# Performance work log

Measured on AMD Instinct MI355X. Metric: run time of the kernel, lower is better.

## Reference

```python
import jax, jax.numpy as jnp
import numpy as np

C = 512
GROUPS = 32
EPS = 1e-5  # torch GroupNorm default


def setup_inputs() -> dict:
    key = jax.random.key(0)
    ks = jax.random.split(key, 11)
    B, H, W = 4, 64, 64
    s = 1.0 / np.sqrt(C)
    inp = {
        "x": jax.random.normal(ks[0], (B, C, H, W), dtype=jnp.float32),
        "gn_scale": jnp.ones((C,), jnp.float32),
        "gn_bias": jnp.zeros((C,), jnp.float32),
        "wq": jax.random.normal(ks[1], (C, C), jnp.float32) * s,
        "bq": jax.random.normal(ks[2], (C,), jnp.float32) * 0.01,
        "wk": jax.random.normal(ks[3], (C, C), jnp.float32) * s,
        "bk": jax.random.normal(ks[4], (C,), jnp.float32) * 0.01,
        "wv": jax.random.normal(ks[5], (C, C), jnp.float32) * s,
        "bv": jax.random.normal(ks[6], (C,), jnp.float32) * 0.01,
        "wo": jax.random.normal(ks[7], (C, C), jnp.float32) * s,
        "bo": jax.random.normal(ks[8], (C,), jnp.float32) * 0.01,
    }
    return inp


def group_norm(x, scale, bias):
    # x: [B, C, H, W]; normalize within each of GROUPS channel groups over (C/G, H, W)
    B, Cc, H, W = x.shape
    xg = x.reshape(B, GROUPS, Cc // GROUPS, H, W)
    mean = jnp.mean(xg, axis=(2, 3, 4), keepdims=True)
    var = jnp.var(xg, axis=(2, 3, 4), keepdims=True)
    xg = (xg - mean) * jax.lax.rsqrt(var + EPS)
    xn = xg.reshape(B, Cc, H, W)
    return xn * scale[None, :, None, None] + bias[None, :, None, None]


def reference(x, gn_scale, gn_bias, wq, bq, wk, bk, wv, bv, wo, bo):
    B, Cc, H, W = x.shape
    h = group_norm(x, gn_scale, gn_bias)
    # 1x1 convs == channel matmuls; work in [B, HW, C] layout
    hf = h.reshape(B, Cc, H * W).transpose(0, 2, 1)  # [B, N, C]
    q = hf @ wq.T + bq                               # [B, N, C]
    k = hf @ wk.T + bk
    v = hf @ wv.T + bv
    scale = jnp.asarray(Cc, x.dtype) ** -0.5
    attn = jnp.einsum("bnc,bmc->bnm", q, k) * scale  # [B, N, N]
    attn = jax.nn.softmax(attn, axis=-1)
    o = jnp.einsum("bnm,bmc->bnc", attn, v)          # [B, N, C]
    o = o @ wo.T + bo
    o = o.transpose(0, 2, 1).reshape(B, Cc, H, W)
    return x + o
```

## Files before the change

### kernel.cpp

```cpp
#include <hip/hip_runtime.h>
#include <cstdint>
#include <cstddef>

typedef unsigned short ushort_t;
typedef __attribute__((ext_vector_type(8))) __bf16 bf16x8;
typedef __attribute__((ext_vector_type(4))) float f32x4;

#define DEVINL __device__ __forceinline__

DEVINL ushort_t f2bf(float f) {
  union { __bf16 b; ushort_t u; } v;
  v.b = (__bf16)f;
  return v.u;
}
DEVINL float bf2f(ushort_t u) {
  union { unsigned u; float f; } v; v.u = ((unsigned)u) << 16;
  return v.f;
}

DEVINL float wred_sum(float x) {
#pragma unroll
  for (int o = 32; o > 0; o >>= 1) x += __shfl_xor(x, o, 64);
  return x;
}

DEVINL void async16(ushort_t* lds, const ushort_t* g) {
  __builtin_amdgcn_global_load_lds(
      (__attribute__((address_space(1))) const unsigned int*)g,
      (__attribute__((address_space(3))) unsigned int*)lds, 16, 0, 0);
}

template <int CPR>
DEVINL int fswz(int r) {
  if constexpr (CPR == 4) return (r >> 2) & 3;
  else return r & 7;
}

__global__ __launch_bounds__(256) void gn_stats_k(const float* __restrict__ x,
                                                  float* __restrict__ stats) {
  const int bg = blockIdx.x;
  const float4* base = (const float4*)(x + ((size_t)bg << 16));
  float s = 0.f, q = 0.f;
  for (int i = threadIdx.x; i < 16384; i += 256) {
    float4 f = base[i];
    s += f.x + f.y + f.z + f.w;
    q += f.x * f.x + f.y * f.y + f.z * f.z + f.w * f.w;
  }
  s = wred_sum(s);
  q = wred_sum(q);
  __shared__ float rs[4], rq[4];
  const int lane = threadIdx.x & 63, wid = threadIdx.x >> 6;
  if (lane == 0) { rs[wid] = s; rq[wid] = q; }
  __syncthreads();
  if (threadIdx.x == 0) {
    float S = rs[0] + rs[1] + rs[2] + rs[3];
    float Q = rq[0] + rq[1] + rq[2] + rq[3];
    float mean = S * (1.f / 65536.f);
    float var = Q * (1.f / 65536.f) - mean * mean;
    stats[2 * bg] = mean;
    stats[2 * bg + 1] = rsqrtf(var + 1e-5f);
  }
}

__global__ __launch_bounds__(256) void gn_apply_k(const float* __restrict__ x,
                                                  const float* __restrict__ stats,
                                                  const float* __restrict__ gs,
                                                  const float* __restrict__ gb,
                                                  ushort_t* __restrict__ h) {
  __shared__ ushort_t tile[32][33];
  const int bid = blockIdx.x;
  const int b = bid >> 11;
  const int r = bid & 2047;
  const int ct = r >> 7, nt = r & 127;
  const int c0 = ct << 5, n0 = nt << 5;
  const int tx = threadIdx.x & 31, ty = threadIdx.x >> 5;
#pragma unroll
  for (int i = 0; i < 4; ++i) {
    const int c = c0 + ty + i * 8;
    const float mean = stats[2 * (b * 32 + (c >> 4))];
    const float rstd = stats[2 * (b * 32 + (c >> 4)) + 1];
    const float xv = x[(((size_t)b * 512 + c) << 12) + n0 + tx];
    tile[ty + i * 8][tx] = f2bf((xv - mean) * rstd * gs[c] + gb[c]);
  }
  __syncthreads();
#pragma unroll
  for (int i = 0; i < 4; ++i) {
    const int n = n0 + ty + i * 8;
    h[(((size_t)b << 12) + n) * 512 + c0 + tx] = tile[tx][ty + i * 8];
  }
}

struct Ptr4 { const float* src[4]; float wsc[4]; };
__global__ __launch_bounds__(256) void cvt_all_k(Ptr4 s, ushort_t* __restrict__ dst) {
  const int i = blockIdx.x * 256 + threadIdx.x;
  const int m = i >> 18;
  dst[i] = f2bf(s.src[m][i & 262143] * s.wsc[m]);
}

struct Ptr3 { const float* bias[3]; ushort_t* out[3]; float bs[3]; };

template <int BM, int BN, int BK, int EPI>
__global__ __launch_bounds__(256) void gemm_nt_k(
    const ushort_t* __restrict__ A, int lda, const ushort_t* __restrict__ Bm, int ldb,
    void* __restrict__ Cout, int ldc, const float* __restrict__ bias,
    const float* __restrict__ resid, float scale, int K,
    size_t azs, size_t bzs, size_t czs, Ptr3 p3, float* __restrict__ lbuf) {
  constexpr int CPR = BK / 8;
  constexpr int WTM = BM / 2, WTN = BN / 2;
  constexpr int MI = WTM / 16, NI = WTN / 16;
  constexpr int AR = (BM * CPR) / 256;
  constexpr int BR = (BN * CPR) / 256;
  __shared__ ushort_t Als[BM * BK];
  __shared__ ushort_t Bls[BN * BK];
  const int tid = threadIdx.x;
  const int lane = tid & 63;
  const int wid = tid >> 6;
  const int quad = lane >> 4;
  const int r16 = lane & 15;
  const int wm = wid >> 1, wn = wid & 1;
  const int m0 = blockIdx.y * BM;
  const int n0 = blockIdx.x * BN;
  const int zb = blockIdx.z;

  A += azs * zb;
  Bm += bzs * zb;

  f32x4 acc[MI][NI] = {};

  for (int kt = 0; kt < K; kt += BK) {
#pragma unroll
    for (int r = 0; r < AR; ++r) {
      const int s = r * 256 + tid;
      const int row = s / CPR;
      const int q = (s % CPR) ^ fswz<CPR>(row);
      async16(&Als[s << 3], A + (size_t)(m0 + row) * lda + kt + (q << 3));
    }
#pragma unroll
    for (int r = 0; r < BR; ++r) {
      const int s = r * 256 + tid;
      const int row = s / CPR;
      const int q = (s % CPR) ^ fswz<CPR>(row);
      async16(&Bls[s << 3], Bm + (size_t)(n0 + row) * ldb + kt + (q << 3));
    }
    __syncthreads();
#pragma unroll
    for (int kf = 0; kf < BK / 32; ++kf) {
      bf16x8 af[MI], bfr[NI];
#pragma unroll
      for (int mi = 0; mi < MI; ++mi) {
        const int lr = wm * WTM + mi * 16 + r16;
        const int ch = kf * 4 + quad;
        af[mi] = *reinterpret_cast<const bf16x8*>(
            &Als[(lr * CPR + (ch ^ fswz<CPR>(lr))) << 3]);
      }
#pragma unroll
      for (int ni = 0; ni < NI; ++ni) {
        const int lr = wn * WTN + ni * 16 + r16;
        const int ch = kf * 4 + quad;
        bfr[ni] = *reinterpret_cast<const bf16x8*>(
            &Bls[(lr * CPR + (ch ^ fswz<CPR>(lr))) << 3]);
      }
#pragma unroll
      for (int mi = 0; mi < MI; ++mi)
#pragma unroll
        for (int ni = 0; ni < NI; ++ni)
          acc[mi][ni] = __builtin_amdgcn_mfma_f32_16x16x32_bf16(
              af[mi], bfr[ni], acc[mi][ni], 0, 0, 0);
    }
    __syncthreads();
  }

  const int mrow = m0 + wm * WTM;
  const int ncol = n0 + wn * WTN;
  if constexpr (EPI == 2) {
    float* C = (float*)Cout;
#pragma unroll
    for (int ni = 0; ni < NI; ++ni) {
      const int col = ncol + ni * 16 + r16;
      const float bvv = bias[col];
#pragma unroll
      for (int mi = 0; mi < MI; ++mi) {
        const int rowb = mrow + mi * 16 + quad * 4;
        const int bb = rowb >> 12;
        const int nl = rowb & 4095;
        const size_t base = (((size_t)bb * 512 + col) << 12) + nl;
        const float4 rv = *(const float4*)&resid[base];
        float4 ov;
        ov.x = rv.x + acc[mi][ni][0] + bvv;
        ov.y = rv.y + acc[mi][ni][1] + bvv;
        ov.z = rv.z + acc[mi][ni][2] + bvv;
        ov.w = rv.w + acc[mi][ni][3] + bvv;
        *(float4*)&C[base] = ov;
      }
    }
  } else if constexpr (EPI == 3) {
    const float* bz = p3.bias[zb];
    const float bsc = p3.bs[zb];
    ushort_t* O = p3.out[zb];
    if (zb < 2) {
#pragma unroll
      for (int ni = 0; ni < NI; ++ni) {
        const int col = ncol + ni * 16 + r16;
        const float bvv = bz[col] * bsc;
#pragma unroll
        for (int mi = 0; mi < MI; ++mi) {
          const int rowb = mrow + mi * 16 + quad * 4;
#pragma unroll
          for (int rr = 0; rr < 4; ++rr)
            O[(size_t)(rowb + rr) * 512 + col] = f2bf(acc[mi][ni][rr] + bvv);
        }
      }
    } else {
#pragma unroll
      for (int ni = 0; ni < NI; ++ni) {
        const int col = ncol + ni * 16 + r16;
        const float bvv = bz[col];
#pragma unroll
        for (int mi = 0; mi < MI; ++mi) {
          const int rowb = mrow + mi * 16 + quad * 4;
          const int bb = rowb >> 12;
          const int nn = rowb & 4095;
          ushort4 pk;
          pk.x = f2bf(acc[mi][ni][0] + bvv);
          pk.y = f2bf(acc[mi][ni][1] + bvv);
          pk.z = f2bf(acc[mi][ni][2] + bvv);
          pk.w = f2bf(acc[mi][ni][3] + bvv);
          *(ushort4*)&O[(((size_t)bb * 512 + col) << 12) + nn] = pk;
        }
      }
    }
  }
}

template <int BM, int BN, int WGM, int WGN, int EPI>
__global__ __launch_bounds__(512, 2) void gemm8p_k(
    const ushort_t* __restrict__ A, int lda,
    const ushort_t* __restrict__ Bm, int ldb,
    void* __restrict__ Cout, int ldc, int K,
    size_t azs, size_t bzs, size_t czs, float* __restrict__ lbuf) {
  constexpr int WTM = BM / WGM, WTN = BN / WGN;
  constexpr int MI = WTM / 16, NI = WTN / 16;
  constexpr int MH = MI / 2, NH = NI / 2;
  constexpr int ALD = BM / 64;
  constexpr int BLD = BN / 64;
  constexpr int TOT = ALD + BLD;
  constexpr int VMC = TOT / 4;
  constexpr int AHALF = BM * 64;
  constexpr int HALF = (BM + BN) * 64;

  extern __shared__ ushort_t lds8[];
  const int tid = threadIdx.x;
  const int lane = tid & 63;
  const int quad = lane >> 4;
  const int r16 = lane & 15;
  const int wid = tid >> 6;
  const int wm = wid / WGN, wn = wid % WGN;

  int bx, by, bz;
  {
    const int flat = blockIdx.x + (EPI == 4 ? 16 : 4) * (blockIdx.y + 16 * blockIdx.z);
    if constexpr (EPI == 4) {
      const int xcd = flat & 7, s = flat >> 3;
      const int w = s & 31, half = w >> 4, idx = w & 15;
      bx = (xcd & 3) * 4 + (idx & 3);
      by = ((xcd >> 2) + 2 * half) * 4 + (idx >> 2);
      bz = s >> 5;
    } else {
      const int xcd = flat & 7, s = flat >> 3;
      bx = s & 3;
      const int yz = xcd + (s >> 2) * 8;
      by = yz & 15; bz = yz >> 4;
    }
  }
  const int m0 = by * BM, n0 = bx * BN, zb = bz;
  A += azs * zb;
  Bm += bzs * zb;
  const int NT = K >> 6;

  const ushort_t* src[TOT];
  ushort_t* dst[TOT];
#pragma unroll
  for (int l = 0; l < TOT; ++l) {
    const bool isA = l < ALD;
    const int li = isA ? l : l - ALD;
    const int s = li * 512 + tid;
    const int row = s >> 3;
    const int q = (s & 7) ^ (row & 7);
    src[l] = (isA ? A + (size_t)(m0 + row) * lda
                  : Bm + (size_t)(n0 + row) * ldb) + (q << 3);
    dst[l] = lds8 + (isA ? 0 : AHALF) + (s << 3);
  }

  f32x4 acc[MI][NI] = {};

#pragma unroll
  for (int l = 0; l < TOT; ++l) async16(dst[l], src[l]);

  bf16x8 afq[MH][2], bfq[NH][2];

#pragma unroll 2
  for (int t = 0; t < NT; ++t) {
    const int nbuf = (t + 1) & 1;
    const ushort_t* Ab = lds8 + (t & 1) * HALF;
    const ushort_t* Bb = Ab + AHALF;
    const int koff = ((t + 1 < NT) ? t + 1 : NT - 1) << 6;

#define STAGEG(G)                                                              \
    { constexpr int S_ = ((G) * TOT) / 4, E_ = (((G) + 1) * TOT) / 4;          \
      _Pragma("unroll")                                                        \
      for (int l = S_; l < E_; ++l) async16(dst[l] + nbuf * HALF, src[l] + koff); }

#define LOADA(MHh)                                                             \
    _Pragma("unroll") for (int i = 0; i < MH; ++i)                             \
    _Pragma("unroll") for (int kf = 0; kf < 2; ++kf) {                         \
      const int lr = wm * WTM + ((MHh) * MH + i) * 16 + r16;                   \
      const int cc = (kf * 4 + quad) ^ (lr & 7);                               \
      afq[i][kf] = *reinterpret_cast<const bf16x8*>(&Ab[lr * 64 + cc * 8]); }

#define LOADB(NHh)                                                             \
    _Pragma("unroll") for (int j = 0; j < NH; ++j)                             \
    _Pragma("unroll") for (int kf = 0; kf < 2; ++kf) {                         \
      const int lr = wn * WTN + ((NHh) * NH + j) * 16 + r16;                   \
      const int cc = (kf * 4 + quad) ^ (lr & 7);                               \
      bfq[j][kf] = *reinterpret_cast<const bf16x8*>(&Bb[lr * 64 + cc * 8]); }

#define MMAQ(MHh, NHh)                                                         \
    __builtin_amdgcn_s_setprio(1);                                             \
    _Pragma("unroll") for (int i = 0; i < MH; ++i)                             \
    _Pragma("unroll") for (int j = 0; j < NH; ++j)                             \
    _Pragma("unroll") for (int kf = 0; kf < 2; ++kf)                           \
      acc[(MHh) * MH + i][(NHh) * NH + j] =                                    \
          __builtin_amdgcn_mfma_f32_16x16x32_bf16(                             \
              afq[i][kf], bfq[j][kf], acc[(MHh) * MH + i][(NHh) * NH + j],     \
              0, 0, 0);                                                        \
    __builtin_amdgcn_s_setprio(0);

    STAGEG(0)
    asm volatile("s_waitcnt vmcnt(%0)" :: "i"(VMC) : "memory");
    __builtin_amdgcn_s_barrier();
    __builtin_amdgcn_sched_barrier(0);
    LOADA(0)
    LOADB(0)
    MMAQ(0, 0)
    __builtin_amdgcn_sched_barrier(0);
    __builtin_amdgcn_s_barrier();
    STAGEG(1)
    LOADB(1)
    MMAQ(0, 1)
    __builtin_amdgcn_sched_barrier(0);
    __builtin_amdgcn_s_barrier();
    STAGEG(2)
    LOADA(1)
    MMAQ(1, 1)
    __builtin_amdgcn_sched_barrier(0);
    __builtin_amdgcn_s_barrier();
    STAGEG(3)
    LOADB(0)
    MMAQ(1, 0)
    __builtin_amdgcn_sched_barrier(0);
    __builtin_amdgcn_s_barrier();
#undef STAGEG
#undef LOADA
#undef LOADB
#undef MMAQ
  }

  const int mrow = m0 + wm * WTM;
  const int ncol = n0 + wn * WTN;
  if constexpr (EPI == 4) {
    ushort_t* C = (ushort_t*)Cout + czs * zb;
    float* Lz = lbuf + (size_t)zb * 4096;
#pragma unroll
    for (int mi = 0; mi < MI; ++mi) {
#pragma unroll
      for (int rr = 0; rr < 4; ++rr) {
        const int row = mrow + mi * 16 + quad * 4 + rr;
        float ps = 0.f;
#pragma unroll
        for (int ni = 0; ni < NI; ++ni) {
          const int col = ncol + ni * 16 + r16;
          const ushort_t ub = f2bf(__expf(acc[mi][ni][rr]));
          C[(size_t)row * ldc + col] = ub;
          ps += bf2f(ub);
        }
#pragma unroll
        for (int o = 1; o < 16; o <<= 1) ps += __shfl_xor(ps, o, 64);
        if (r16 == 0) atomicAdd(&Lz[row], ps);
      }
    }
  } else {
    ushort_t* C = (ushort_t*)Cout + czs * zb;
    const float* Lz = lbuf + (size_t)zb * 4096;
#pragma unroll
    for (int mi = 0; mi < MI; ++mi) {
#pragma unroll
      for (int rr = 0; rr < 4; ++rr) {
        const int row = mrow + mi * 16 + quad * 4 + rr;
        const float inv = 1.f / Lz[row];
#pragma unroll
        for (int ni = 0; ni < NI; ++ni) {
          const int col = ncol + ni * 16 + r16;
          C[(size_t)row * ldc + col] = f2bf(acc[mi][ni][rr] * inv);
        }
      }
    }
  }
}

extern "C" void kernel_launch(void* const* d_in, const int* in_sizes, int n_in,
                              void* d_out, int out_size, void* d_ws, size_t ws_size,
                              hipStream_t stream) {
  const float* x  = (const float*)d_in[0];
  const float* gs = (const float*)d_in[1];
  const float* gb = (const float*)d_in[2];
  const float* wq = (const float*)d_in[3];
  const float* bq = (const float*)d_in[4];
  const float* wk = (const float*)d_in[5];
  const float* bk = (const float*)d_in[6];
  const float* wv = (const float*)d_in[7];
  const float* bv = (const float*)d_in[8];
  const float* wo = (const float*)d_in[9];
  const float* bo = (const float*)d_in[10];
  float* out = (float*)d_out;

  const size_t HNC = (size_t)4 * 4096 * 512;
  char* w = (char*)d_ws;
  float* stats  = (float*)w;    w += 4096;
  float* Ls     = (float*)w;    w += (size_t)4 * 4096 * 4;
  ushort_t* wb  = (ushort_t*)w; w += (size_t)4 * 262144 * 2;
  ushort_t* h   = (ushort_t*)w; w += HNC * 2;
  ushort_t* q   = (ushort_t*)w; w += HNC * 2;
  ushort_t* kk  = (ushort_t*)w; w += HNC * 2;
  ushort_t* vt  = (ushort_t*)w; w += HNC * 2;
  ushort_t* Se  = (ushort_t*)w; w += (size_t)4 * 4096 * 4096 * 2;

  const float sc = 0.044194173824159216f;

  static bool attr_done = false;
  if (!attr_done) {
    (void)hipFuncSetAttribute((const void*)gemm8p_k<256, 256, 2, 4, 4>,
                              hipFuncAttributeMaxDynamicSharedMemorySize, 131072);
    (void)hipFuncSetAttribute((const void*)gemm8p_k<256, 128, 4, 2, 5>,
                              hipFuncAttributeMaxDynamicSharedMemorySize, 98304);
    attr_done = true;
  }

  gn_stats_k<<<128, 256, 0, stream>>>(x, stats);
  gn_apply_k<<<8192, 256, 0, stream>>>(x, stats, gs, gb, h);
  Ptr4 wsrc;
  wsrc.src[0] = wq; wsrc.src[1] = wk; wsrc.src[2] = wv; wsrc.src[3] = wo;
  wsrc.wsc[0] = sc; wsrc.wsc[1] = 1.f; wsrc.wsc[2] = 1.f; wsrc.wsc[3] = 1.f;
  cvt_all_k<<<4096, 256, 0, stream>>>(wsrc, wb);
  hipMemsetAsync(Ls, 0, (size_t)4 * 4096 * 4, stream);

  Ptr3 qkv;
  qkv.bias[0] = bq; qkv.bias[1] = bk; qkv.bias[2] = bv;
  qkv.out[0] = q; qkv.out[1] = kk; qkv.out[2] = vt;
  qkv.bs[0] = sc; qkv.bs[1] = 1.f; qkv.bs[2] = 1.f;
  gemm_nt_k<128, 128, 32, 3><<<dim3(4, 128, 3), 256, 0, stream>>>(
      h, 512, wb, 512, nullptr, 0, nullptr, nullptr, 1.f, 512,
      0, 262144, 0, qkv, nullptr);

  gemm8p_k<256, 256, 2, 4, 4><<<dim3(16, 16, 4), 512, 131072, stream>>>(
      q, 512, kk, 512, Se, 4096, 512,
      (size_t)4096 * 512, (size_t)4096 * 512, (size_t)4096 * 4096, Ls);
  gemm8p_k<256, 128, 4, 2, 5><<<dim3(4, 16, 4), 512, 98304, stream>>>(
      Se, 4096, vt, 4096, h, 512, 4096,
      (size_t)4096 * 4096, (size_t)512 * 4096, (size_t)4096 * 512, Ls);

  Ptr3 e0{};
  gemm_nt_k<128, 128, 32, 2><<<dim3(4, 128, 1), 256, 0, stream>>>(
      h, 512, wb + (size_t)3 * 262144, 512, out, 512, bo, x, 1.f, 512,
      0, 0, 0, e0, nullptr);
}
```

Before: 394.7 us.

## Compute softmax row sums via ones-MFMA in PV GEMM, drop atomics and memset

The softmax denominator is no longer accumulated with per-row atomicAdds in the QK^T epilogue. Instead the PV GEMM runs extra MFMAs against a vector of ones to sum the exp'd bf16 scores per row, and the memset and L buffer go away. The finely staged 4-phase ping-pong main loop with partial vmcnt waits is also replaced by a simpler loop: full vmcnt/lgkmcnt wait, one barrier per K-step, all B fragments held in registers. This removes atomic traffic but adds MFMA work and register pressure, and may lose the latency hiding the old staged schedule provided.

```diff
diff --git a/kernel.cpp b/kernel.cpp
--- a/kernel.cpp
+++ b/kernel.cpp
@@ -104,7 +104,7 @@
     const ushort_t* __restrict__ A, int lda, const ushort_t* __restrict__ Bm, int ldb,
     void* __restrict__ Cout, int ldc, const float* __restrict__ bias,
     const float* __restrict__ resid, float scale, int K,
-    size_t azs, size_t bzs, size_t czs, Ptr3 p3, float* __restrict__ lbuf) {
+    size_t azs, size_t bzs, size_t czs, Ptr3 p3) {
   constexpr int CPR = BK / 8;
   constexpr int WTM = BM / 2, WTN = BN / 2;
   constexpr int MI = WTM / 16, NI = WTN / 16;
@@ -233,18 +233,17 @@
 }
 
 template <int BM, int BN, int WGM, int WGN, int EPI>
-__global__ __launch_bounds__(512, 2) void gemm8p_k(
+__global__ __launch_bounds__(512, 2) void gemm8l_k(
     const ushort_t* __restrict__ A, int lda,
     const ushort_t* __restrict__ Bm, int ldb,
     void* __restrict__ Cout, int ldc, int K,
-    size_t azs, size_t bzs, size_t czs, float* __restrict__ lbuf) {
+    size_t azs, size_t bzs, size_t czs) {
   constexpr int WTM = BM / WGM, WTN = BN / WGN;
   constexpr int MI = WTM / 16, NI = WTN / 16;
-  constexpr int MH = MI / 2, NH = NI / 2;
+  constexpr int MH = MI / 2;
   constexpr int ALD = BM / 64;
   constexpr int BLD = BN / 64;
   constexpr int TOT = ALD + BLD;
-  constexpr int VMC = TOT / 4;
   constexpr int AHALF = BM * 64;
   constexpr int HALF = (BM + BN) * 64;
 
@@ -278,7 +277,7 @@
   const int NT = K >> 6;
 
   const ushort_t* src[TOT];
-  ushort_t* dst[TOT];
+  int dsto[TOT];
 #pragma unroll
   for (int l = 0; l < TOT; ++l) {
     const bool isA = l < ALD;
@@ -288,115 +287,99 @@
     const int q = (s & 7) ^ (row & 7);
     src[l] = (isA ? A + (size_t)(m0 + row) * lda
                   : Bm + (size_t)(n0 + row) * ldb) + (q << 3);
-    dst[l] = lds8 + (isA ? 0 : AHALF) + (s << 3);
+    dsto[l] = (isA ? 0 : AHALF) + (s << 3);
   }
 
   f32x4 acc[MI][NI] = {};
-
-#pragma unroll
-  for (int l = 0; l < TOT; ++l) async16(dst[l], src[l]);
-
-  bf16x8 afq[MH][2], bfq[NH][2];
-
-#pragma unroll 2
+  f32x4 acc_l[MI] = {};
+  bf16x8 ones;
+  {
+    union { ushort_t u; __bf16 b; } o1; o1.u = 0x3F80;
+#pragma unroll
+    for (int j = 0; j < 8; ++j) ones[j] = o1.b;
+  }
+
+#pragma unroll
+  for (int l = 0; l < TOT; ++l) async16(lds8 + dsto[l], src[l]);
+
   for (int t = 0; t < NT; ++t) {
     const int nbuf = (t + 1) & 1;
     const ushort_t* Ab = lds8 + (t & 1) * HALF;
     const ushort_t* Bb = Ab + AHALF;
     const int koff = ((t + 1 < NT) ? t + 1 : NT - 1) << 6;
 
-#define STAGEG(G)                                                              \
-    { constexpr int S_ = ((G) * TOT) / 4, E_ = (((G) + 1) * TOT) / 4;          \
-      _Pragma("unroll")                                                        \
-      for (int l = S_; l < E_; ++l) async16(dst[l] + nbuf * HALF, src[l] + koff); }
-
-#define LOADA(MHh)                                                             \
-    _Pragma("unroll") for (int i = 0; i < MH; ++i)                             \
-    _Pragma("unroll") for (int kf = 0; kf < 2; ++kf) {                         \
-      const int lr = wm * WTM + ((MHh) * MH + i) * 16 + r16;                   \
-      const int cc = (kf * 4 + quad) ^ (lr & 7);                               \
-      afq[i][kf] = *reinterpret_cast<const bf16x8*>(&Ab[lr * 64 + cc * 8]); }
-
-#define LOADB(NHh)                                                             \
-    _Pragma("unroll") for (int j = 0; j < NH; ++j)                             \
-    _Pragma("unroll") for (int kf = 0; kf < 2; ++kf) {                         \
-      const int lr = wn * WTN + ((NHh) * NH + j) * 16 + r16;                   \
-      const int cc = (kf * 4 + quad) ^ (lr & 7);                               \
-      bfq[j][kf] = *reinterpret_cast<const bf16x8*>(&Bb[lr * 64 + cc * 8]); }
-
-#define MMAQ(MHh, NHh)                                                         \
-    __builtin_amdgcn_s_setprio(1);                                             \
-    _Pragma("unroll") for (int i = 0; i < MH; ++i)                             \
-    _Pragma("unroll") for (int j = 0; j < NH; ++j)                             \
-    _Pragma("unroll") for (int kf = 0; kf < 2; ++kf)                           \
-      acc[(MHh) * MH + i][(NHh) * NH + j] =                                    \
-          __builtin_amdgcn_mfma_f32_16x16x32_bf16(                             \
-              afq[i][kf], bfq[j][kf], acc[(MHh) * MH + i][(NHh) * NH + j],     \
-              0, 0, 0);                                                        \
-    __builtin_amdgcn_s_setprio(0);
-
-    STAGEG(0)
-    asm volatile("s_waitcnt vmcnt(%0)" :: "i"(VMC) : "memory");
+    asm volatile("s_waitcnt vmcnt(0) lgkmcnt(0)" ::: "memory");
     __builtin_amdgcn_s_barrier();
-    __builtin_amdgcn_sched_barrier(0);
-    LOADA(0)
-    LOADB(0)
-    MMAQ(0, 0)
-    __builtin_amdgcn_sched_barrier(0);
-    __builtin_amdgcn_s_barrier();
-    STAGEG(1)
-    LOADB(1)
-    MMAQ(0, 1)
-    __builtin_amdgcn_sched_barrier(0);
-    __builtin_amdgcn_s_barrier();
-    STAGEG(2)
-    LOADA(1)
-    MMAQ(1, 1)
-    __builtin_amdgcn_sched_barrier(0);
-    __builtin_amdgcn_s_barrier();
-    STAGEG(3)
-    LOADB(0)
-    MMAQ(1, 0)
-    __builtin_amdgcn_sched_barrier(0);
-    __builtin_amdgcn_s_barrier();
-#undef STAGEG
-#undef LOADA
-#undef LOADB
-#undef MMAQ
-  }
+
+#pragma unroll
+    for (int l = 0; l < TOT; ++l)
+      async16(lds8 + nbuf * HALF + dsto[l], src[l] + koff);
+
+    bf16x8 bfr[NI][2], af[MH][2];
+#pragma unroll
+    for (int ni = 0; ni < NI; ++ni)
+#pragma unroll
+      for (int kf = 0; kf < 2; ++kf) {
+        const int lr = wn * WTN + ni * 16 + r16;
+        const int cc = (kf * 4 + quad) ^ (lr & 7);
+        bfr[ni][kf] = *reinterpret_cast<const bf16x8*>(&Bb[lr * 64 + cc * 8]);
+      }
+#pragma unroll
+    for (int h = 0; h < 2; ++h) {
+#pragma unroll
+      for (int i = 0; i < MH; ++i)
+#pragma unroll
+        for (int kf = 0; kf < 2; ++kf) {
+          const int lr = wm * WTM + (h * MH + i) * 16 + r16;
+          const int cc = (kf * 4 + quad) ^ (lr & 7);
+          af[i][kf] = *reinterpret_cast<const bf16x8*>(&Ab[lr * 64 + cc * 8]);
+        }
+      __builtin_amdgcn_s_setprio(1);
+#pragma unroll
+      for (int i = 0; i < MH; ++i)
+#pragma unroll
+        for (int ni = 0; ni < NI; ++ni)
+#pragma unroll
+          for (int kf = 0; kf < 2; ++kf)
+            acc[h * MH + i][ni] = __builtin_amdgcn_mfma_f32_16x16x32_bf16(
+                af[i][kf], bfr[ni][kf], acc[h * MH + i][ni], 0, 0, 0);
+      if constexpr (EPI == 5) {
+#pragma unroll
+        for (int i = 0; i < MH; ++i)
+#pragma unroll
+          for (int kf = 0; kf < 2; ++kf)
+            acc_l[h * MH + i] = __builtin_amdgcn_mfma_f32_16x16x32_bf16(
+                af[i][kf], ones, acc_l[h * MH + i], 0, 0, 0);
+      }
+      __builtin_amdgcn_s_setprio(0);
+    }
+  }
+  asm volatile("s_waitcnt vmcnt(0)" ::: "memory");
 
   const int mrow = m0 + wm * WTM;
   const int ncol = n0 + wn * WTN;
   if constexpr (EPI == 4) {
     ushort_t* C = (ushort_t*)Cout + czs * zb;
-    float* Lz = lbuf + (size_t)zb * 4096;
 #pragma unroll
     for (int mi = 0; mi < MI; ++mi) {
 #pragma unroll
       for (int rr = 0; rr < 4; ++rr) {
         const int row = mrow + mi * 16 + quad * 4 + rr;
-        float ps = 0.f;
 #pragma unroll
         for (int ni = 0; ni < NI; ++ni) {
           const int col = ncol + ni * 16 + r16;
-          const ushort_t ub = f2bf(__expf(acc[mi][ni][rr]));
-          C[(size_t)row * ldc + col] = ub;
-          ps += bf2f(ub);
+          C[(size_t)row * ldc + col] = f2bf(__expf(acc[mi][ni][rr]));
         }
-#pragma unroll
-        for (int o = 1; o < 16; o <<= 1) ps += __shfl_xor(ps, o, 64);
-        if (r16 == 0) atomicAdd(&Lz[row], ps);
       }
     }
   } else {
     ushort_t* C = (ushort_t*)Cout + czs * zb;
-    const float* Lz = lbuf + (size_t)zb * 4096;
 #pragma unroll
     for (int mi = 0; mi < MI; ++mi) {
 #pragma unroll
       for (int rr = 0; rr < 4; ++rr) {
         const int row = mrow + mi * 16 + quad * 4 + rr;
-        const float inv = 1.f / Lz[row];
+        const float inv = 1.f / acc_l[mi][rr];
 #pragma unroll
         for (int ni = 0; ni < NI; ++ni) {
           const int col = ncol + ni * 16 + r16;
@@ -426,7 +409,6 @@
   const size_t HNC = (size_t)4 * 4096 * 512;
   char* w = (char*)d_ws;
   float* stats  = (float*)w;    w += 4096;
-  float* Ls     = (float*)w;    w += (size_t)4 * 4096 * 4;
   ushort_t* wb  = (ushort_t*)w; w += (size_t)4 * 262144 * 2;
   ushort_t* h   = (ushort_t*)w; w += HNC * 2;
   ushort_t* q   = (ushort_t*)w; w += HNC * 2;
@@ -438,9 +420,9 @@
 
   static bool attr_done = false;
   if (!attr_done) {
-    (void)hipFuncSetAttribute((const void*)gemm8p_k<256, 256, 2, 4, 4>,
+    (void)hipFuncSetAttribute((const void*)gemm8l_k<256, 256, 2, 4, 4>,
                               hipFuncAttributeMaxDynamicSharedMemorySize, 131072);
-    (void)hipFuncSetAttribute((const void*)gemm8p_k<256, 128, 4, 2, 5>,
+    (void)hipFuncSetAttribute((const void*)gemm8l_k<256, 128, 4, 2, 5>,
                               hipFuncAttributeMaxDynamicSharedMemorySize, 98304);
     attr_done = true;
   }
@@ -451,7 +433,6 @@
   wsrc.src[0] = wq; wsrc.src[1] = wk; wsrc.src[2] = wv; wsrc.src[3] = wo;
   wsrc.wsc[0] = sc; wsrc.wsc[1] = 1.f; wsrc.wsc[2] = 1.f; wsrc.wsc[3] = 1.f;
   cvt_all_k<<<4096, 256, 0, stream>>>(wsrc, wb);
-  hipMemsetAsync(Ls, 0, (size_t)4 * 4096 * 4, stream);
 
   Ptr3 qkv;
   qkv.bias[0] = bq; qkv.bias[1] = bk; qkv.bias[2] = bv;
@@ -459,17 +440,17 @@
   qkv.bs[0] = sc; qkv.bs[1] = 1.f; qkv.bs[2] = 1.f;
   gemm_nt_k<128, 128, 32, 3><<<dim3(4, 128, 3), 256, 0, stream>>>(
       h, 512, wb, 512, nullptr, 0, nullptr, nullptr, 1.f, 512,
-      0, 262144, 0, qkv, nullptr);
-
-  gemm8p_k<256, 256, 2, 4, 4><<<dim3(16, 16, 4), 512, 131072, stream>>>(
+      0, 262144, 0, qkv);
+
+  gemm8l_k<256, 256, 2, 4, 4><<<dim3(16, 16, 4), 512, 131072, stream>>>(
       q, 512, kk, 512, Se, 4096, 512,
-      (size_t)4096 * 512, (size_t)4096 * 512, (size_t)4096 * 4096, Ls);
-  gemm8p_k<256, 128, 4, 2, 5><<<dim3(4, 16, 4), 512, 98304, stream>>>(
+      (size_t)4096 * 512, (size_t)4096 * 512, (size_t)4096 * 4096);
+  gemm8l_k<256, 128, 4, 2, 5><<<dim3(4, 16, 4), 512, 98304, stream>>>(
       Se, 4096, vt, 4096, h, 512, 4096,
-      (size_t)4096 * 4096, (size_t)512 * 4096, (size_t)4096 * 512, Ls);
+      (size_t)4096 * 4096, (size_t)512 * 4096, (size_t)4096 * 512);
 
   Ptr3 e0{};
   gemm_nt_k<128, 128, 32, 2><<<dim3(4, 128, 1), 256, 0, stream>>>(
       h, 512, wb + (size_t)3 * 262144, 512, out, 512, bo, x, 1.f, 512,
-      0, 0, 0, e0, nullptr);
-}
+      0, 0, 0, e0);
+}
```

Measured after the change: 353.4 us. 10.5% less time.
